# Optimization experiments

Hardware: AMD Instinct MI355X
Metric: run time of the kernel (lower is better)

## Reference

```python
import jax, jax.numpy as jnp
import numpy as np

SIZE = 11
SIGMA = 1.5
C1 = 0.01 ** 2
C2 = 0.03 ** 2


def gaussian_kernel(size, sigma):
    x, y = np.mgrid[-size:size + 1, -size:size + 1]
    k = np.exp(-0.5 * (x * x + y * y) / (sigma * sigma))
    return (k / k.sum()).astype(np.float32)


def _dwconv(x, w, pad):
    # depthwise conv, NCHW input, OIHW kernel (C,1,kh,kw)
    return jax.lax.conv_general_dilated(
        x, w, window_strides=(1, 1), padding=[(pad, pad), (pad, pad)],
        dimension_numbers=('NCHW', 'OIHW', 'NCHW'),
        feature_group_count=x.shape[1])


def setup_inputs() -> dict:
    key = jax.random.key(0)
    k1, k2 = jax.random.split(key)
    B, C, H, W = 16, 3, 512, 512
    inp = jax.random.uniform(k1, (B, C, H, W), dtype=jnp.float32)
    tgt = jax.random.uniform(k2, (B, C, H, W), dtype=jnp.float32)
    kern = gaussian_kernel(SIZE, SIGMA)  # (23,23)
    weight = jnp.asarray(np.tile(kern, (C, 1, 1, 1)))  # (C,1,23,23)
    return {"input": inp, "target": tgt, "weight": weight}


def reference(input, target, weight):
    pad = SIZE
    mean1 = _dwconv(input, weight, pad)
    mean2 = _dwconv(target, weight, pad)
    mean1_sq = mean1 * mean1
    mean2_sq = mean2 * mean2
    mean_12 = mean1 * mean2
    sigma1_sq = _dwconv(input * input, weight, pad) - mean1_sq
    sigma2_sq = _dwconv(target * target, weight, pad) - mean2_sq
    sigma_12 = _dwconv(input * target, weight, pad) - mean_12
    ssim = (2 * mean_12 + C1) * (2 * sigma_12 + C2) / (
        (mean1_sq + mean2_sq + C1) * (sigma1_sq + sigma2_sq + C2))
    return 1.0 - ssim.mean()
```

## Files before the change

### kernel.cpp

```cpp
#include <hip/hip_runtime.h>
#include <hip/hip_bf16.h>

typedef float f32x4 __attribute__((ext_vector_type(4)));
typedef float f32x2 __attribute__((ext_vector_type(2)));
typedef _Float16 f16x8 __attribute__((ext_vector_type(8)));
typedef _Float16 f16x2 __attribute__((ext_vector_type(2)));
typedef __fp16 h16x2 __attribute__((ext_vector_type(2)));

#define HH 512
#define WW 512
#define NPLANES 48
#define KSIZE 23
#define NBLK (16 * 16 * NPLANES)
#define C1V 1.0e-4f
#define C2V 9.0e-4f

#define SB_O   0
#define SA_O   3960
#define OV_O   7920
#define G_O    8568
#define HB_O   0
#define HB_CH  2048
#define SPITCH 72
#define LDS_TOT 10616

#define SWZ(rho, k) ((k) ^ (((rho) & 7) << 3))

__device__ __forceinline__ unsigned cvtpk(float a, float b) {
    union { h16x2 h; unsigned u; } cv;
    cv.h = __builtin_amdgcn_cvt_pkrtz(a, b);
    return cv.u;
}

__device__ __forceinline__ void prod2(unsigned a, unsigned b,
                                      unsigned& pab, unsigned& pss) {
    union U { f16x2 h; unsigned u; } ua, ub, r1, r2;
    ua.u = a; ub.u = b;
    r1.h = ua.h * ub.h;
    r2.h = ua.h * ua.h + ub.h * ub.h;
    pab = r1.u; pss = r2.u;
}

__device__ __forceinline__ f32x4 mfma16(uint4 a, uint4 b, f32x4 c) {
    union { uint4 u; f16x8 h; } ua, ub;
    ua.u = a; ub.u = b;
    return __builtin_amdgcn_mfma_f32_16x16x32_f16(ua.h, ub.h, c, 0, 0, 0);
}

__global__ __launch_bounds__(64) void ssim_prep_kernel(
    const float* __restrict__ w, unsigned* __restrict__ Gg)
{
    const int lane = threadIdx.x;
    float gv = 0.f;
    if (lane < KSIZE) {
        #pragma unroll
        for (int k = 0; k < KSIZE; ++k) gv += w[lane * KSIZE + k];
    }
    for (int idx = lane; idx < 32 * 32; idx += 64) {
        int r = idx >> 5, kd = idx & 31;
        int d0 = 2 * kd - 1 - r;
        float g0 = __shfl(gv, d0 & 63, 64);
        float g1 = __shfl(gv, (d0 + 1) & 63, 64);
        g0 = ((unsigned)d0 < (unsigned)KSIZE) ? g0 : 0.f;
        g1 = ((unsigned)(d0 + 1) < (unsigned)KSIZE) ? g1 : 0.f;
        Gg[idx] = cvtpk(g0, g1);
    }
}

__global__ __launch_bounds__(256, 7) void ssim_main_kernel(
    const float* __restrict__ in, const float* __restrict__ tg,
    const unsigned* __restrict__ Gg, float* __restrict__ partial)
{
    __shared__ __align__(16) unsigned short lds[LDS_TOT];
    __shared__ float swsum[4];

    const int tid = threadIdx.x;
    const int wave = tid >> 6, lane = tid & 63;
    const int m = lane & 15, q = lane >> 4;

    const int blk = (blockIdx.x & 7) * (NBLK / 8) + (blockIdx.x >> 3);
    const int plane = blk >> 8;
    const int t2 = blk & 255;
    const int x0 = (t2 & 15) * 32 - 12;
    const int y0 = (t2 >> 4) * 32 - 12;
    const float* __restrict__ inp = in + (size_t)plane * (HH * WW);
    const float* __restrict__ tgp = tg + (size_t)plane * (HH * WW);

    const bool interior = (x0 >= 0) && (y0 >= 0) && (x0 + 64 <= WW) && (y0 + 55 <= HH);

    float4 La[2][2], Lb[2][2];
    if (interior) {
        #pragma unroll
        for (int it = 0; it < 2; ++it) {
            int t = tid + it * 256;
            if (t < 440) {
                int r = t >> 3, c8 = (t & 7) << 3;
                const float4* pa = (const float4*)(inp + (y0 + r) * WW + x0 + c8);
                const float4* pb = (const float4*)(tgp + (y0 + r) * WW + x0 + c8);
                La[it][0] = pa[0]; La[it][1] = pa[1];
                Lb[it][0] = pb[0]; Lb[it][1] = pb[1];
            }
        }
    }

    {
        int r = tid >> 3;
        int dc = (tid & 7) << 2;
        uint4 g4 = *(const uint4*)(Gg + r * 32 + dc);
        *(uint4*)&lds[G_O + r * 64 + (((dc << 1)) ^ ((r & 7) << 3))] = g4;
    }
    if (tid < 81) {
        uint4 z; z.x = z.y = z.z = z.w = 0u;
        *(uint4*)&lds[OV_O + tid * 8] = z;
    }

    if (interior) {
        #pragma unroll
        for (int it = 0; it < 2; ++it) {
            int t = tid + it * 256;
            if (t < 440) {
                int r = t >> 3, c8 = (t & 7) << 3;
                uint4 va, vb;
                va.x = cvtpk(La[it][0].x, La[it][0].y); va.y = cvtpk(La[it][0].z, La[it][0].w);
                va.z = cvtpk(La[it][1].x, La[it][1].y); va.w = cvtpk(La[it][1].z, La[it][1].w);
                vb.x = cvtpk(Lb[it][0].x, Lb[it][0].y); vb.y = cvtpk(Lb[it][0].z, Lb[it][0].w);
                vb.z = cvtpk(Lb[it][1].x, Lb[it][1].y); vb.w = cvtpk(Lb[it][1].z, Lb[it][1].w);
                *(uint4*)&lds[SA_O + r * SPITCH + c8] = va;
                *(uint4*)&lds[SB_O + r * SPITCH + c8] = vb;
            }
        }
    } else {
        unsigned* ldsw = (unsigned*)lds;
        for (int t = tid; t < 55 * 32; t += 256) {
            int r = t >> 5, cd = t & 31;
            int gy = y0 + r, gx = x0 + cd * 2;
            float a0 = 0.f, a1 = 0.f, b0 = 0.f, b1 = 0.f;
            if (gy >= 0 && gy < HH) {
                const float* ri = inp + gy * WW;
                const float* rt = tgp + gy * WW;
                if ((unsigned)gx < (unsigned)WW)       { a0 = ri[gx];     b0 = rt[gx]; }
                if ((unsigned)(gx + 1) < (unsigned)WW) { a1 = ri[gx + 1]; b1 = rt[gx + 1]; }
            }
            ldsw[(SA_O >> 1) + r * 36 + cd] = cvtpk(a0, a1);
            ldsw[(SB_O >> 1) + r * 36 + cd] = cvtpk(b0, b1);
        }
    }
    __syncthreads();

    f32x4 acc[4][2];
    const f32x4 zz = {0.f, 0.f, 0.f, 0.f};
    #pragma unroll
    for (int ch = 0; ch < 4; ++ch) { acc[ch][0] = zz; acc[ch][1] = zz; }

    #pragma unroll
    for (int ks = 0; ks < 2; ++ks) {
        const int off = (wave * 16 + m) * SPITCH + ks * 32 + q * 8;
        uint4 ua = *(const uint4*)&lds[SA_O + off];
        uint4 ub = *(const uint4*)&lds[SB_O + off];
        uint4 uab, uss;
        prod2(ua.x, ub.x, uab.x, uss.x);
        prod2(ua.y, ub.y, uab.y, uss.y);
        prod2(ua.z, ub.z, uab.z, uss.z);
        prod2(ua.w, ub.w, uab.w, uss.w);
        #pragma unroll
        for (int nc = 0; nc < 2; ++nc) {
            const int gr = nc * 16 + m;
            uint4 gf = *(const uint4*)&lds[G_O + gr * 64 + SWZ(gr, ks * 32 + q * 8)];
            acc[0][nc] = mfma16(ua,  gf, acc[0][nc]);
            acc[1][nc] = mfma16(ub,  gf, acc[1][nc]);
            acc[2][nc] = mfma16(uss, gf, acc[2][nc]);
            acc[3][nc] = mfma16(uab, gf, acc[3][nc]);
        }
    }
    __syncthreads();

    #pragma unroll
    for (int ch = 0; ch < 4; ++ch)
        #pragma unroll
        for (int nc = 0; nc < 2; ++nc) {
            f32x4 a = acc[ch][nc];
            uint2 pk;
            pk.x = cvtpk(a[0], a[1]);
            pk.y = cvtpk(a[2], a[3]);
            const int col = nc * 16 + m;
            const int rb = wave * 16 + q * 4;
            *(uint2*)&lds[HB_O + ch * HB_CH + col * 64 + SWZ(col, rb)] = pk;
        }
    __syncthreads();

    const int mrow = wave >> 1, nc2 = wave & 1;
    f32x4 av[4];
    #pragma unroll
    for (int ch = 0; ch < 4; ++ch) av[ch] = zz;

    #pragma unroll
    for (int ks = 0; ks < 2; ++ks) {
        const int ar = mrow * 16 + m;
        uint4 ga = *(const uint4*)&lds[G_O + ar * 64 + SWZ(ar, ks * 32 + q * 8)];
        #pragma unroll
        for (int ch = 0; ch < 4; ++ch) {
            const int col = nc2 * 16 + m;
            uint4 ub = *(const uint4*)&lds[HB_O + ch * HB_CH + col * 64 + SWZ(col, ks * 32 + q * 8)];
            av[ch] = mfma16(ga, ub, av[ch]);
        }
    }

    float nacc[2], dacc[2];
    #pragma unroll
    for (int h = 0; h < 2; ++h) {
        f32x2 vx  = {av[0][2 * h], av[0][2 * h + 1]};
        f32x2 vt  = {av[1][2 * h], av[1][2 * h + 1]};
        f32x2 vss = {av[2][2 * h], av[2][2 * h + 1]};
        f32x2 vxt = {av[3][2 * h], av[3][2 * h + 1]};
        f32x2 m1s = vx * vx, m2s = vt * vt, m12 = vx * vt;
        f32x2 p   = m1s + m2s;
        f32x2 s12 = vxt - m12;
        f32x2 num = (2.f * m12 + C1V) * (2.f * s12 + C2V);
        f32x2 den = (p + C1V) * ((vss + C2V) - p);
        nacc[h] = num[0] * den[1] + num[1] * den[0];
        dacc[h] = den[0] * den[1];
    }
    float nn = nacc[0] * dacc[1] + nacc[1] * dacc[0];
    float dd = dacc[0] * dacc[1];
    float lsum = nn * __builtin_amdgcn_rcpf(dd);

    #pragma unroll
    for (int off = 32; off > 0; off >>= 1)
        lsum += __shfl_down(lsum, off, 64);
    if (lane == 0) swsum[wave] = lsum;
    __syncthreads();
    if (tid == 0)
        partial[blk] = swsum[0] + swsum[1] + swsum[2] + swsum[3];
}

__global__ __launch_bounds__(256) void ssim_final_kernel(
    const float* __restrict__ partial, float* __restrict__ out)
{
    __shared__ float swsum[4];
    const int tid = threadIdx.x;
    float s = 0.f;
    const float4* p4 = (const float4*)partial;
    for (int i = tid; i < NBLK / 4; i += 256) {
        float4 v = p4[i];
        s += (v.x + v.y) + (v.z + v.w);
    }
    #pragma unroll
    for (int off = 32; off > 0; off >>= 1)
        s += __shfl_down(s, off, 64);
    if ((tid & 63) == 0) swsum[tid >> 6] = s;
    __syncthreads();
    if (tid == 0)
        out[0] = 1.0f - (swsum[0] + swsum[1] + swsum[2] + swsum[3])
                        * (1.0f / ((float)NPLANES * HH * WW));
}

extern "C" void kernel_launch(void* const* d_in, const int* in_sizes, int n_in,
                              void* d_out, int out_size, void* d_ws, size_t ws_size,
                              hipStream_t stream) {
    const float* inp = (const float*)d_in[0];
    const float* tgt = (const float*)d_in[1];
    const float* wgt = (const float*)d_in[2];
    float* out = (float*)d_out;
    float* partial = (float*)d_ws;
    unsigned* Gg = (unsigned*)((char*)d_ws + NBLK * sizeof(float));

    ssim_prep_kernel<<<1, 64, 0, stream>>>(wgt, Gg);
    ssim_main_kernel<<<NBLK, 256, 0, stream>>>(inp, tgt, Gg, partial);
    ssim_final_kernel<<<1, 256, 0, stream>>>(partial, out);
}
```

Measured before the change: 148.7 us.

## Load input tiles straight into MFMA fragment registers, skipping LDS staging

Each lane now reads its own rows and columns of input and target straight from global memory as float4s and converts them to fp16 in registers for the horizontal MFMA pass. The LDS staging buffers, the separate interior and border load paths, and one barrier are removed, and LDS use shrinks. Global loads are now narrower per lane and less coalesced, and partial border float4s are zeroed as whole vectors, which may mishandle edge columns. Launch bounds drop from 7 to 6 blocks per SM.

```diff
diff --git a/kernel.cpp b/kernel.cpp
--- a/kernel.cpp
+++ b/kernel.cpp
@@ -15,14 +15,10 @@
 #define C1V 1.0e-4f
 #define C2V 9.0e-4f
 
-#define SB_O   0
-#define SA_O   3960
-#define OV_O   7920
-#define G_O    8568
 #define HB_O   0
 #define HB_CH  2048
-#define SPITCH 72
-#define LDS_TOT 10616
+#define G_O    8192
+#define LDS_TOT 10240
 
 #define SWZ(rho, k) ((k) ^ (((rho) & 7) << 3))
 
@@ -67,7 +63,7 @@
     }
 }
 
-__global__ __launch_bounds__(256, 7) void ssim_main_kernel(
+__global__ __launch_bounds__(256, 6) void ssim_main_kernel(
     const float* __restrict__ in, const float* __restrict__ tg,
     const unsigned* __restrict__ Gg, float* __restrict__ partial)
 {
@@ -86,65 +82,27 @@
     const float* __restrict__ inp = in + (size_t)plane * (HH * WW);
     const float* __restrict__ tgp = tg + (size_t)plane * (HH * WW);
 
-    const bool interior = (x0 >= 0) && (y0 >= 0) && (x0 + 64 <= WW) && (y0 + 55 <= HH);
-
-    float4 La[2][2], Lb[2][2];
-    if (interior) {
-        #pragma unroll
-        for (int it = 0; it < 2; ++it) {
-            int t = tid + it * 256;
-            if (t < 440) {
-                int r = t >> 3, c8 = (t & 7) << 3;
-                const float4* pa = (const float4*)(inp + (y0 + r) * WW + x0 + c8);
-                const float4* pb = (const float4*)(tgp + (y0 + r) * WW + x0 + c8);
-                La[it][0] = pa[0]; La[it][1] = pa[1];
-                Lb[it][0] = pb[0]; Lb[it][1] = pb[1];
-            }
-        }
-    }
-
-    {
-        int r = tid >> 3;
-        int dc = (tid & 7) << 2;
-        uint4 g4 = *(const uint4*)(Gg + r * 32 + dc);
-        *(uint4*)&lds[G_O + r * 64 + (((dc << 1)) ^ ((r & 7) << 3))] = g4;
-    }
-    if (tid < 81) {
-        uint4 z; z.x = z.y = z.z = z.w = 0u;
-        *(uint4*)&lds[OV_O + tid * 8] = z;
-    }
-
-    if (interior) {
-        #pragma unroll
-        for (int it = 0; it < 2; ++it) {
-            int t = tid + it * 256;
-            if (t < 440) {
-                int r = t >> 3, c8 = (t & 7) << 3;
-                uint4 va, vb;
-                va.x = cvtpk(La[it][0].x, La[it][0].y); va.y = cvtpk(La[it][0].z, La[it][0].w);
-                va.z = cvtpk(La[it][1].x, La[it][1].y); va.w = cvtpk(La[it][1].z, La[it][1].w);
-                vb.x = cvtpk(Lb[it][0].x, Lb[it][0].y); vb.y = cvtpk(Lb[it][0].z, Lb[it][0].w);
-                vb.z = cvtpk(Lb[it][1].x, Lb[it][1].y); vb.w = cvtpk(Lb[it][1].z, Lb[it][1].w);
-                *(uint4*)&lds[SA_O + r * SPITCH + c8] = va;
-                *(uint4*)&lds[SB_O + r * SPITCH + c8] = vb;
-            }
-        }
-    } else {
-        unsigned* ldsw = (unsigned*)lds;
-        for (int t = tid; t < 55 * 32; t += 256) {
-            int r = t >> 5, cd = t & 31;
-            int gy = y0 + r, gx = x0 + cd * 2;
-            float a0 = 0.f, a1 = 0.f, b0 = 0.f, b1 = 0.f;
-            if (gy >= 0 && gy < HH) {
-                const float* ri = inp + gy * WW;
-                const float* rt = tgp + gy * WW;
-                if ((unsigned)gx < (unsigned)WW)       { a0 = ri[gx];     b0 = rt[gx]; }
-                if ((unsigned)(gx + 1) < (unsigned)WW) { a1 = ri[gx + 1]; b1 = rt[gx + 1]; }
-            }
-            ldsw[(SA_O >> 1) + r * 36 + cd] = cvtpk(a0, a1);
-            ldsw[(SB_O >> 1) + r * 36 + cd] = cvtpk(b0, b1);
-        }
-    }
+    const int gr_ = tid >> 3;
+    const int gdc = (tid & 7) << 2;
+    uint4 g4 = *(const uint4*)(Gg + gr_ * 32 + gdc);
+
+    const int gy = y0 + wave * 16 + m;
+    const bool rowOK = ((unsigned)gy < (unsigned)HH);
+    const float* __restrict__ ri = inp + gy * WW;
+    const float* __restrict__ rt = tgp + gy * WW;
+    const float4 z4 = {0.f, 0.f, 0.f, 0.f};
+    float4 fa[2][2], fb[2][2];
+    #pragma unroll
+    for (int ks = 0; ks < 2; ++ks)
+        #pragma unroll
+        for (int sg = 0; sg < 2; ++sg) {
+            const int cb = x0 + ks * 32 + q * 8 + sg * 4;
+            const bool ok = rowOK && ((unsigned)cb <= (unsigned)(WW - 4));
+            fa[ks][sg] = ok ? *(const float4*)(ri + cb) : z4;
+            fb[ks][sg] = ok ? *(const float4*)(rt + cb) : z4;
+        }
+
+    *(uint4*)&lds[G_O + gr_ * 64 + ((gdc << 1) ^ ((gr_ & 7) << 3))] = g4;
     __syncthreads();
 
     f32x4 acc[4][2];
@@ -154,9 +112,11 @@
 
     #pragma unroll
     for (int ks = 0; ks < 2; ++ks) {
-        const int off = (wave * 16 + m) * SPITCH + ks * 32 + q * 8;
-        uint4 ua = *(const uint4*)&lds[SA_O + off];
-        uint4 ub = *(const uint4*)&lds[SB_O + off];
+        uint4 ua, ub;
+        ua.x = cvtpk(fa[ks][0].x, fa[ks][0].y); ua.y = cvtpk(fa[ks][0].z, fa[ks][0].w);
+        ua.z = cvtpk(fa[ks][1].x, fa[ks][1].y); ua.w = cvtpk(fa[ks][1].z, fa[ks][1].w);
+        ub.x = cvtpk(fb[ks][0].x, fb[ks][0].y); ub.y = cvtpk(fb[ks][0].z, fb[ks][0].w);
+        ub.z = cvtpk(fb[ks][1].x, fb[ks][1].y); ub.w = cvtpk(fb[ks][1].z, fb[ks][1].w);
         uint4 uab, uss;
         prod2(ua.x, ub.x, uab.x, uss.x);
         prod2(ua.y, ub.y, uab.y, uss.y);
@@ -172,7 +132,6 @@
             acc[3][nc] = mfma16(uab, gf, acc[3][nc]);
         }
     }
-    __syncthreads();
 
     #pragma unroll
     for (int ch = 0; ch < 4; ++ch)
```

New measurement: 274.7 us. +84.7%, slower.
